# Optimization experiments

Measured on AMD Instinct MI355X. Metric: run time of the kernel, lower is better.

Reference implementation:

```python
import jax, jax.numpy as jnp
import numpy as np

B, N, D, DA = 8, 2048, 512, 64


def setup_inputs() -> dict:
    key = jax.random.key(0)
    ks = jax.random.split(key, 10)
    s = 1.0 / np.sqrt(D)
    return {
        "x": jax.random.normal(ks[0], (B, N, D), jnp.float32),
        "query_aux": jax.random.normal(ks[1], (B, N, DA), jnp.float32),
        "key_aux": jax.random.normal(ks[2], (B, N, DA), jnp.float32),
        "adjacency_mask": jax.random.randint(ks[3], (B, N, N), 0, 2, jnp.int32),
        "merge_coefficients": jax.random.uniform(ks[4], (1,), jnp.float32),
        "Wq": jax.random.normal(ks[5], (D, D), jnp.float32) * s,
        "bq": jnp.zeros((D,), jnp.float32),
        "Wk": jax.random.normal(ks[6], (D, D), jnp.float32) * s,
        "bk": jnp.zeros((D,), jnp.float32),
        "Wv": jax.random.normal(ks[7], (D, D), jnp.float32) * s,
        "bv": jnp.zeros((D,), jnp.float32),
        "threshold": jnp.float32(0.5),
    }


def reference(x, query_aux, key_aux, adjacency_mask, merge_coefficients,
              Wq, bq, Wk, bk, Wv, bv, threshold):
    d_model = Wq.shape[0]
    scale = jnp.asarray(d_model, x.dtype) ** 0.5
    # torch nn.Linear: y = x @ W.T + b
    q = jnp.einsum('bnd,ed->bne', x, Wq) + bq
    k = jnp.einsum('bnd,ed->bne', x, Wk) + bk
    v = jnp.einsum('bnd,ed->bne', x, Wv) + bv

    scores = jnp.einsum('bne,bme->bnm', q, k) / scale  # [B,N,N]

    aux_scale = jnp.asarray(key_aux.shape[-1], x.dtype) ** 0.5
    scores_aux = jnp.einsum('bna,bma->bnm', query_aux, key_aux) / aux_scale

    merge_mask = (scores_aux != 0) & (scores > threshold)
    c = merge_coefficients
    merged = (1.0 - c) * scores + c * scores_aux
    scores = jnp.where(merge_mask, merged, scores)

    mask_value = jnp.finfo(scores.dtype).min
    scores = jnp.where(adjacency_mask == 0, mask_value, scores)

    weights = jax.nn.softmax(scores, axis=-1)
    return jnp.einsum('bnm,bme->bne', weights, v)
```

## Files before the change

### kernel.cpp

```cpp
#include <hip/hip_runtime.h>
#include <cstdint>

typedef _Float16 f16;
typedef _Float16 f16x4 __attribute__((ext_vector_type(4)));
typedef _Float16 f16x8 __attribute__((ext_vector_type(8)));
typedef float    f32x4 __attribute__((ext_vector_type(4)));

#define MFMA(a,b,c) __builtin_amdgcn_mfma_f32_16x16x32_f16((a),(b),(c),0,0,0)

constexpr int  Bb = 8, Nn = 2048, Dd = 512, Ad = 64;
constexpr long XN = (long)Bb*Nn*Dd;
constexpr long WN = (long)Dd*Dd;
constexpr long AN = (long)Bb*Nn*Ad;
constexpr float LO_S  = 4096.f;
constexpr float LO_INV= 1.f/4096.f;
constexpr float P_SC  = 1024.f;
constexpr float NEGF  = -3.402823466e38f;

__global__ void prep_split(const float* __restrict__ x,
  const float* __restrict__ Wq, const float* __restrict__ Wk, const float* __restrict__ Wv,
  const float* __restrict__ aq, const float* __restrict__ ak,
  f16* __restrict__ xh, f16* __restrict__ xl, f16* __restrict__ Wh, f16* __restrict__ Wl,
  f16* __restrict__ aqh, f16* __restrict__ akh)
{
  const long total4 = (XN + 3*WN + 2*AN) >> 2;
  for (long u = blockIdx.x*(long)blockDim.x + threadIdx.x; u < total4;
       u += (long)gridDim.x*blockDim.x) {
    long i = u << 2;
    if (i < XN) {
      float4 v = *(const float4*)(x + i);
      float vv[4] = {v.x, v.y, v.z, v.w};
      f16x4 h, l;
      #pragma unroll
      for (int t=0;t<4;++t){ f16 hh=(f16)vv[t]; h[t]=hh; l[t]=(f16)((vv[t]-(float)hh)*LO_S); }
      *(f16x4*)(xh+i)=h; *(f16x4*)(xl+i)=l;
    } else if (i < XN + 3*WN) {
      long j = i - XN;
      const float* w = (j < WN) ? (Wq + j) : (j < 2*WN ? (Wk + (j-WN)) : (Wv + (j-2*WN)));
      float4 v = *(const float4*)w;
      float vv[4] = {v.x, v.y, v.z, v.w};
      f16x4 h, l;
      #pragma unroll
      for (int t=0;t<4;++t){ f16 hh=(f16)vv[t]; h[t]=hh; l[t]=(f16)((vv[t]-(float)hh)*LO_S); }
      *(f16x4*)(Wh+j)=h; *(f16x4*)(Wl+j)=l;
    } else {
      long j = i - XN - 3*WN;
      const float* s = (j < AN) ? (aq + j) : (ak + (j-AN));
      f16*         d = (j < AN) ? (aqh + j) : (akh + (j-AN));
      float4 v = *(const float4*)s;
      float vv[4] = {v.x, v.y, v.z, v.w};
      f16x4 h;
      #pragma unroll
      for (int t=0;t<4;++t) h[t]=(f16)vv[t];
      *(f16x4*)d = h;
    }
  }
}

__global__ __launch_bounds__(256, 2) void proj_qk(
  const f16* __restrict__ xh, const f16* __restrict__ xl,
  const f16* __restrict__ Wh, const f16* __restrict__ Wl,
  const float* __restrict__ bq, const float* __restrict__ bk,
  f16* __restrict__ qh, f16* __restrict__ ql,
  f16* __restrict__ kh, f16* __restrict__ kl)
{
  const int z = blockIdx.z;
  const f16* Whz = Wh + (long)z*WN;
  const f16* Wlz = Wl + (long)z*WN;
  const float* bias = z ? bk : bq;
  f16* oh = z ? kh : qh;
  f16* ol = z ? kl : ql;
  const int e0 = blockIdx.x*128, m0 = blockIdx.y*128;
  __shared__ f16 Ah[128][40], Al[128][40], Bh[128][40], Bl[128][40];
  const int tid = threadIdx.x, lane = tid & 63, wid = tid >> 6;
  const int wi = wid & 1, wj = wid >> 1;
  const int r16 = lane & 15, g16 = lane >> 4;

  f32x4 acch[4][4], accl[4][4];
  #pragma unroll
  for (int a=0;a<4;++a)
    #pragma unroll
    for (int bI=0;bI<4;++bI){ acch[a][bI]=(f32x4){0.f,0.f,0.f,0.f}; accl[a][bI]=(f32x4){0.f,0.f,0.f,0.f}; }

  f16x8 st[8];
  #pragma unroll
  for (int t=0;t<2;++t) {
    int u = tid + t*256; int row = u>>2, sg = u&3;
    long ko = (long)sg*8;
    st[t*4+0] = *(const f16x8*)&Whz[(long)(e0+row)*Dd + ko];
    st[t*4+1] = *(const f16x8*)&Wlz[(long)(e0+row)*Dd + ko];
    st[t*4+2] = *(const f16x8*)&xh [(long)(m0+row)*Dd + ko];
    st[t*4+3] = *(const f16x8*)&xl [(long)(m0+row)*Dd + ko];
  }
  for (int kt=0; kt<16; ++kt) {
    __syncthreads();
    #pragma unroll
    for (int t=0;t<2;++t) {
      int u = tid + t*256; int row = u>>2, sg = u&3;
      *(f16x8*)&Ah[row][sg*8] = st[t*4+0];
      *(f16x8*)&Al[row][sg*8] = st[t*4+1];
      *(f16x8*)&Bh[row][sg*8] = st[t*4+2];
      *(f16x8*)&Bl[row][sg*8] = st[t*4+3];
    }
    __syncthreads();
    if (kt < 15) {
      #pragma unroll
      for (int t=0;t<2;++t) {
        int u = tid + t*256; int row = u>>2, sg = u&3;
        long ko = (long)(kt+1)*32 + sg*8;
        st[t*4+0] = *(const f16x8*)&Whz[(long)(e0+row)*Dd + ko];
        st[t*4+1] = *(const f16x8*)&Wlz[(long)(e0+row)*Dd + ko];
        st[t*4+2] = *(const f16x8*)&xh [(long)(m0+row)*Dd + ko];
        st[t*4+3] = *(const f16x8*)&xl [(long)(m0+row)*Dd + ko];
      }
    }
    f16x8 ahf[4], alf[4];
    #pragma unroll
    for (int fi=0;fi<4;++fi) {
      ahf[fi] = *(const f16x8*)&Ah[wi*64 + fi*16 + r16][g16*8];
      alf[fi] = *(const f16x8*)&Al[wi*64 + fi*16 + r16][g16*8];
    }
    #pragma unroll
    for (int fj=0;fj<4;++fj) {
      f16x8 bhf = *(const f16x8*)&Bh[wj*64 + fj*16 + r16][g16*8];
      f16x8 blf = *(const f16x8*)&Bl[wj*64 + fj*16 + r16][g16*8];
      #pragma unroll
      for (int fi=0;fi<4;++fi) {
        acch[fi][fj] = MFMA(ahf[fi], bhf, acch[fi][fj]);
        accl[fi][fj] = MFMA(ahf[fi], blf, accl[fi][fj]);
        accl[fi][fj] = MFMA(alf[fi], bhf, accl[fi][fj]);
      }
    }
  }
  #pragma unroll
  for (int fi=0;fi<4;++fi) {
    const int eb = e0 + wi*64 + fi*16 + g16*4;
    const float4 b4 = *(const float4*)&bias[eb];
    const float bbv[4] = {b4.x, b4.y, b4.z, b4.w};
    #pragma unroll
    for (int fj=0;fj<4;++fj) {
      const int xr = m0 + wj*64 + fj*16 + r16;
      f16x4 h4, l4;
      #pragma unroll
      for (int rg=0;rg<4;++rg) {
        float v = acch[fi][fj][rg] + accl[fi][fj][rg]*LO_INV + bbv[rg];
        f16 hh = (f16)v;
        h4[rg] = hh;
        l4[rg] = (f16)((v - (float)hh)*LO_S);
      }
      *(f16x4*)&oh[(long)xr*Dd + eb] = h4;
      *(f16x4*)&ol[(long)xr*Dd + eb] = l4;
    }
  }
}

__global__ __launch_bounds__(256, 2) void proj_v(
  const f16* __restrict__ xh, const f16* __restrict__ Wvh,
  const float* __restrict__ bv, f16* __restrict__ vT)
{
  const int e0 = blockIdx.x*128, m0 = blockIdx.y*128;
  __shared__ f16 Ax[128][40], Bw[128][40];
  const int tid = threadIdx.x, lane = tid & 63, wid = tid >> 6;
  const int wi = wid & 1, wj = wid >> 1;
  const int r16 = lane & 15, g16 = lane >> 4;

  f32x4 acc[4][4];
  #pragma unroll
  for (int a=0;a<4;++a)
    #pragma unroll
    for (int bI=0;bI<4;++bI) acc[a][bI]=(f32x4){0.f,0.f,0.f,0.f};

  f16x8 st[4];
  #pragma unroll
  for (int t=0;t<2;++t) {
    int u = tid + t*256; int row = u>>2, sg = u&3;
    st[t*2+0] = *(const f16x8*)&xh [(long)(m0+row)*Dd + sg*8];
    st[t*2+1] = *(const f16x8*)&Wvh[(long)(e0+row)*Dd + sg*8];
  }
  for (int kt=0; kt<16; ++kt) {
    __syncthreads();
    #pragma unroll
    for (int t=0;t<2;++t) {
      int u = tid + t*256; int row = u>>2, sg = u&3;
      *(f16x8*)&Ax[row][sg*8] = st[t*2+0];
      *(f16x8*)&Bw[row][sg*8] = st[t*2+1];
    }
    __syncthreads();
    if (kt < 15) {
      #pragma unroll
      for (int t=0;t<2;++t) {
        int u = tid + t*256; int row = u>>2, sg = u&3;
        long ko = (long)(kt+1)*32 + sg*8;
        st[t*2+0] = *(const f16x8*)&xh [(long)(m0+row)*Dd + ko];
        st[t*2+1] = *(const f16x8*)&Wvh[(long)(e0+row)*Dd + ko];
      }
    }
    f16x8 af[4];
    #pragma unroll
    for (int fi=0;fi<4;++fi) af[fi] = *(const f16x8*)&Ax[wi*64 + fi*16 + r16][g16*8];
    #pragma unroll
    for (int fj=0;fj<4;++fj) {
      f16x8 bf = *(const f16x8*)&Bw[wj*64 + fj*16 + r16][g16*8];
      #pragma unroll
      for (int fi=0;fi<4;++fi) acc[fi][fj] = MFMA(af[fi], bf, acc[fi][fj]);
    }
  }
  #pragma unroll
  for (int fj=0;fj<4;++fj) {
    const int e = e0 + wj*64 + fj*16 + r16;
    const float bve = bv[e];
    #pragma unroll
    for (int fi=0;fi<4;++fi) {
      const int xr0 = m0 + wi*64 + fi*16 + g16*4;
      const int bbi = xr0 >> 11, nn = xr0 & 2047;
      f16x4 h4;
      #pragma unroll
      for (int rg=0;rg<4;++rg) h4[rg] = (f16)(acc[fi][fj][rg] + bve);
      *(f16x4*)&vT[((long)bbi*Dd + e)*Nn + nn] = h4;
    }
  }
}

constexpr int FLASH_LDS = 121856;

__global__ __launch_bounds__(512, 2) void flash(
  const f16* __restrict__ qhg, const f16* __restrict__ qlg,
  const f16* __restrict__ khg, const f16* __restrict__ klg,
  const f16* __restrict__ vT,  const f16* __restrict__ aqg, const f16* __restrict__ akg,
  const int* __restrict__ adj, const float* __restrict__ mcp, const float* __restrict__ thp,
  float* __restrict__ out)
{
  extern __shared__ char smem[];
  f16 (* __restrict__ QL)[520] = (f16(*)[520])(smem);
  f16 (* __restrict__ KH)[136] = (f16(*)[136])(smem + 66560);
  f16 (* __restrict__ KL)[136] = (f16(*)[136])(smem + 83968);
  f16 (* __restrict__ AK)[72]  = (f16(*)[72]) (smem + 101376);
  f16 (* __restrict__ PS)[72]  = (f16(*)[72]) (smem + 110592);
  float* pmax = (float*)(smem + 119808);
  float* psum = (float*)(smem + 120320);
  float* mnew = (float*)(smem + 120832);
  float* scl  = (float*)(smem + 121088);
  float* mst  = (float*)(smem + 121344);
  float* lst  = (float*)(smem + 121600);

  const int b  = blockIdx.y;
  const int r0 = blockIdx.x * 64;
  const int tid = threadIdx.x;
  const int lane = tid & 63, wid = tid >> 6;
  const int wm = wid & 3, wn = wid >> 2;
  const int r16 = lane & 15, g16 = lane >> 4;
  const float cc = mcp[0], thr = thp[0];

  if (tid < 64) { mst[tid] = NEGF; lst[tid] = 0.f; }

  const long qbase = ((long)(b*Nn + r0))*Dd;
  for (int u = tid; u < 64*Dd/8; u += 512) {
    int row = u >> 6, sg = u & 63;
    *(f16x8*)&QL[row][sg*8] = *(const f16x8*)&qlg[qbase + (long)row*Dd + sg*8];
  }
  f16x8 qhr[16];
  {
    const f16* qrow = qhg + qbase + (long)(wm*16 + r16)*Dd;
    #pragma unroll
    for (int ks=0; ks<16; ++ks) qhr[ks] = *(const f16x8*)&qrow[ks*32 + g16*8];
  }
  f16x8 aqr[2];
  {
    const f16* arow = aqg + ((long)(b*Nn + r0 + wm*16 + r16))*Ad;
    aqr[0] = *(const f16x8*)&arow[g16*8];
    aqr[1] = *(const f16x8*)&arow[32 + g16*8];
  }
  f32x4 oacc[4][4];
  #pragma unroll
  for (int i=0;i<4;++i)
    #pragma unroll
    for (int j=0;j<4;++j) oacc[i][j] = (f32x4){0.f,0.f,0.f,0.f};

  __syncthreads();

  for (int ct=0; ct<Nn/64; ++ct) {
    const int cb = ct*64;
    int adjv[2][4];
    {
      const int* ap = adj + ((long)(b*Nn + r0 + wm*16))*Nn + cb + wn*32 + r16;
      #pragma unroll
      for (int nf=0; nf<2; ++nf)
        #pragma unroll
        for (int rg=0; rg<4; ++rg)
          adjv[nf][rg] = ap[(long)(g16*4+rg)*Nn + nf*16];
    }
    f32x4 sacc[2], slo[2], aacc[2];
    #pragma unroll
    for (int nf=0;nf<2;++nf){ sacc[nf]=(f32x4){0.f,0.f,0.f,0.f}; slo[nf]=(f32x4){0.f,0.f,0.f,0.f}; aacc[nf]=(f32x4){0.f,0.f,0.f,0.f}; }

    for (int kc=0; kc<4; ++kc) {
      __syncthreads();
      {
        const long gb = ((long)(b*Nn + cb))*Dd + kc*128;
        const int ua = tid, ub = tid + 512;
        const int ra = ua>>4, sa = ua&15, rb = ub>>4, sb = ub&15;
        f16x8 h0 = *(const f16x8*)&khg[gb + (long)ra*Dd + sa*8];
        f16x8 h1 = *(const f16x8*)&khg[gb + (long)rb*Dd + sb*8];
        f16x8 l0 = *(const f16x8*)&klg[gb + (long)ra*Dd + sa*8];
        f16x8 l1 = *(const f16x8*)&klg[gb + (long)rb*Dd + sb*8];
        *(f16x8*)&KH[ra][sa*8] = h0;
        *(f16x8*)&KH[rb][sb*8] = h1;
        *(f16x8*)&KL[ra][sa*8] = l0;
        *(f16x8*)&KL[rb][sb*8] = l1;
        if (kc == 3) {
          int rr = tid>>3, sg = tid&7;
          *(f16x8*)&AK[rr][sg*8] = *(const f16x8*)&akg[((long)(b*Nn + cb))*Ad + (long)rr*Ad + sg*8];
        }
      }
      __syncthreads();
      #pragma unroll
      for (int k4=0; k4<4; ++k4) {
        const int ks = kc*4 + k4;
        f16x8 alo = *(const f16x8*)&QL[wm*16 + r16][ks*32 + g16*8];
        #pragma unroll
        for (int nf=0; nf<2; ++nf) {
          const int cr = wn*32 + nf*16 + r16;
          f16x8 bh = *(const f16x8*)&KH[cr][k4*32 + g16*8];
          f16x8 bl = *(const f16x8*)&KL[cr][k4*32 + g16*8];
          sacc[nf] = MFMA(qhr[ks], bh, sacc[nf]);
          slo[nf]  = MFMA(qhr[ks], bl, slo[nf]);
          slo[nf]  = MFMA(alo,     bh, slo[nf]);
        }
      }
    }
    #pragma unroll
    for (int ks=0; ks<2; ++ks)
      #pragma unroll
      for (int nf=0; nf<2; ++nf) {
        f16x8 bf = *(const f16x8*)&AK[wn*32 + nf*16 + r16][ks*32 + g16*8];
        aacc[nf] = MFMA(aqr[ks], bf, aacc[nf]);
      }
    float sv[2][4], mx[4];
    #pragma unroll
    for (int rg=0; rg<4; ++rg) {
      #pragma unroll
      for (int nf=0; nf<2; ++nf) {
        float s = (sacc[nf][rg] + slo[nf][rg]*LO_INV) / 22.627416997969522f;
        float a = aacc[nf][rg] * 0.125f;
        float m = (1.f - cc)*s + cc*a;
        s = ((a != 0.f) && (s > thr)) ? m : s;
        sv[nf][rg] = adjv[nf][rg] ? s : NEGF;
      }
      mx[rg] = fmaxf(sv[0][rg], sv[1][rg]);
    }
    #pragma unroll
    for (int off=1; off<16; off<<=1)
      #pragma unroll
      for (int rg=0; rg<4; ++rg)
        mx[rg] = fmaxf(mx[rg], __shfl_xor(mx[rg], off));
    if (r16 == 0) {
      #pragma unroll
      for (int rg=0; rg<4; ++rg) pmax[wn*64 + wm*16 + g16*4 + rg] = mx[rg];
    }
    __syncthreads();
    if (tid < 64) {
      float tmax = fmaxf(pmax[tid], pmax[64+tid]);
      float mo = mst[tid];
      float mn = fmaxf(mo, tmax);
      mnew[tid] = mn;
      scl[tid]  = expf(mo - mn);
      mst[tid]  = mn;
    }
    __syncthreads();
    float sm[4];
    #pragma unroll
    for (int rg=0; rg<4; ++rg) {
      const int rr = wm*16 + g16*4 + rg;
      const float mn = mnew[rr];
      float p0 = expf(sv[0][rg] - mn);
      float p1 = expf(sv[1][rg] - mn);
      PS[rr][wn*32 + r16]      = (f16)(p0 * P_SC);
      PS[rr][wn*32 + 16 + r16] = (f16)(p1 * P_SC);
      sm[rg] = p0 + p1;
    }
    #pragma unroll
    for (int off=1; off<16; off<<=1)
      #pragma unroll
      for (int rg=0; rg<4; ++rg)
        sm[rg] += __shfl_xor(sm[rg], off);
    if (r16 == 0) {
      #pragma unroll
      for (int rg=0; rg<4; ++rg) psum[wn*64 + wm*16 + g16*4 + rg] = sm[rg];
    }
    __syncthreads();
    if (tid < 64) lst[tid] = lst[tid]*scl[tid] + psum[tid] + psum[64+tid];
    float scj[4];
    #pragma unroll
    for (int j=0;j<4;++j) scj[j] = scl[j*16 + r16];
    #pragma unroll
    for (int i=0;i<4;++i)
      #pragma unroll
      for (int j=0;j<4;++j)
        #pragma unroll
        for (int rg=0;rg<4;++rg) oacc[i][j][rg] *= scj[j];
    #pragma unroll
    for (int ks=0; ks<2; ++ks) {
      f16x8 va[4];
      const f16* vb = vT + ((long)(b*Dd) + wid*64 + r16)*Nn + cb + ks*32 + g16*8;
      #pragma unroll
      for (int i=0;i<4;++i) va[i] = *(const f16x8*)&vb[(long)i*16*Nn];
      #pragma unroll
      for (int j=0;j<4;++j) {
        f16x8 pb = *(const f16x8*)&PS[j*16 + r16][ks*32 + g16*8];
        #pragma unroll
        for (int i=0;i<4;++i) oacc[i][j] = MFMA(va[i], pb, oacc[i][j]);
      }
    }
  }
  __syncthreads();
  const long ob = ((long)(b*Nn + r0))*Dd;
  #pragma unroll
  for (int j=0;j<4;++j) {
    const int rr = j*16 + r16;
    const float li = 1.f / (lst[rr] * P_SC);
    #pragma unroll
    for (int i=0;i<4;++i) {
      f32x4 v;
      #pragma unroll
      for (int rg=0;rg<4;++rg) v[rg] = oacc[i][j][rg] * li;
      *(f32x4*)&out[ob + (long)rr*Dd + wid*64 + i*16 + g16*4] = v;
    }
  }
}

extern "C" void kernel_launch(void* const* d_in, const int* in_sizes, int n_in,
                              void* d_out, int out_size, void* d_ws, size_t ws_size,
                              hipStream_t stream)
{
  const float* x   = (const float*)d_in[0];
  const float* qa  = (const float*)d_in[1];
  const float* ka  = (const float*)d_in[2];
  const int*   adj = (const int*)  d_in[3];
  const float* mc  = (const float*)d_in[4];
  const float* Wq  = (const float*)d_in[5];
  const float* bq  = (const float*)d_in[6];
  const float* Wk  = (const float*)d_in[7];
  const float* bk  = (const float*)d_in[8];
  const float* Wv  = (const float*)d_in[9];
  const float* bv  = (const float*)d_in[10];
  const float* th  = (const float*)d_in[11];
  float* out = (float*)d_out;

  f16* p  = (f16*)d_ws;
  f16* xh = p;  p += XN;
  f16* xl = p;  p += XN;
  f16* Wh = p;  p += 3*WN;
  f16* Wl = p;  p += 3*WN;
  f16* qh = p;  p += XN;
  f16* ql = p;  p += XN;
  f16* kh = p;  p += XN;
  f16* kl = p;  p += XN;
  f16* vT = p;  p += XN;
  f16* aqh = p; p += AN;
  f16* akh = p; p += AN;

  prep_split<<<dim3(2048), dim3(256), 0, stream>>>(x, Wq, Wk, Wv, qa, ka,
                                                   xh, xl, Wh, Wl, aqh, akh);
  proj_qk<<<dim3(4,128,2), dim3(256), 0, stream>>>(xh, xl, Wh, Wl, bq, bk,
                                                   qh, ql, kh, kl);
  proj_v<<<dim3(4,128), dim3(256), 0, stream>>>(xh, Wh + 2*WN, bv, vT);

  hipFuncSetAttribute(reinterpret_cast<const void*>(flash),
                      hipFuncAttributeMaxDynamicSharedMemorySize, FLASH_LDS);
  flash<<<dim3(Nn/64, Bb), dim3(512), FLASH_LDS, stream>>>(qh, ql, kh, kl, vT,
                                                           aqh, akh, adj, mc, th, out);
}
```

Before: 431.6 us.

## Double-buffer K tiles with register prefetch and swizzled LDS in flash kernel

Prefetches the next K hi/lo chunk into registers during MFMA work and writes it to a second LDS buffer, halving barriers per chunk. Replaces padded LDS arrays with XOR-swizzled layouts, hoists V loads before the softmax, raises wave priority around MFMA blocks, and uses fast exp. The grid is flattened with batch interleaving. Higher LDS use and register pressure may limit occupancy.

```diff
diff --git a/kernel.cpp b/kernel.cpp
--- a/kernel.cpp
+++ b/kernel.cpp
@@ -16,6 +16,9 @@
 constexpr float LO_INV= 1.f/4096.f;
 constexpr float P_SC  = 1024.f;
 constexpr float NEGF  = -3.402823466e38f;
+
+#define QSWZ(row, cb2) ((row)*1024 + ((cb2) ^ (((row)&7)<<4)))
+#define KSWZ(row, cb2) ((row)*256  + ((cb2) ^ (((row)&7)<<4)))
 
 __global__ void prep_split(const float* __restrict__ x,
   const float* __restrict__ Wq, const float* __restrict__ Wk, const float* __restrict__ Wv,
@@ -221,7 +224,7 @@
   }
 }
 
-constexpr int FLASH_LDS = 121856;
+constexpr int FLASH_LDS = 151552;
 
 __global__ __launch_bounds__(512, 2) void flash(
   const f16* __restrict__ qhg, const f16* __restrict__ qlg,
@@ -231,42 +234,47 @@
   float* __restrict__ out)
 {
   extern __shared__ char smem[];
-  f16 (* __restrict__ QL)[520] = (f16(*)[520])(smem);
-  f16 (* __restrict__ KH)[136] = (f16(*)[136])(smem + 66560);
-  f16 (* __restrict__ KL)[136] = (f16(*)[136])(smem + 83968);
-  f16 (* __restrict__ AK)[72]  = (f16(*)[72]) (smem + 101376);
-  f16 (* __restrict__ PS)[72]  = (f16(*)[72]) (smem + 110592);
-  float* pmax = (float*)(smem + 119808);
-  float* psum = (float*)(smem + 120320);
-  float* mnew = (float*)(smem + 120832);
-  float* scl  = (float*)(smem + 121088);
-  float* mst  = (float*)(smem + 121344);
-  float* lst  = (float*)(smem + 121600);
-
-  const int b  = blockIdx.y;
-  const int r0 = blockIdx.x * 64;
+  char* QLb = smem;
+  char* KHb0 = smem + 65536;
+  char* KHb1 = smem + 81920;
+  char* KLb0 = smem + 98304;
+  char* KLb1 = smem + 114688;
+  f16 (* __restrict__ AK)[72] = (f16(*)[72])(smem + 131072);
+  f16 (* __restrict__ PS)[72] = (f16(*)[72])(smem + 140288);
+  float* pmax = (float*)(smem + 149504);
+  float* psum = pmax + 128;
+  float* mnew = psum + 128;
+  float* scl  = mnew + 64;
+  float* mst  = scl + 64;
+  float* lst  = mst + 64;
+
+  const int bid = blockIdx.x;
+  const int b   = bid & 7;
+  const int r0  = (bid >> 3) * 64;
   const int tid = threadIdx.x;
   const int lane = tid & 63, wid = tid >> 6;
   const int wm = wid & 3, wn = wid >> 2;
   const int r16 = lane & 15, g16 = lane >> 4;
+  const int g16c = g16 * 16;
+  const int qrow = wm*16 + r16;
   const float cc = mcp[0], thr = thp[0];
 
   if (tid < 64) { mst[tid] = NEGF; lst[tid] = 0.f; }
 
   const long qbase = ((long)(b*Nn + r0))*Dd;
-  for (int u = tid; u < 64*Dd/8; u += 512) {
+  for (int u = tid; u < 4096; u += 512) {
     int row = u >> 6, sg = u & 63;
-    *(f16x8*)&QL[row][sg*8] = *(const f16x8*)&qlg[qbase + (long)row*Dd + sg*8];
+    *(f16x8*)(QLb + QSWZ(row, sg*16)) = *(const f16x8*)&qlg[qbase + (long)row*Dd + sg*8];
   }
   f16x8 qhr[16];
   {
-    const f16* qrow = qhg + qbase + (long)(wm*16 + r16)*Dd;
-    #pragma unroll
-    for (int ks=0; ks<16; ++ks) qhr[ks] = *(const f16x8*)&qrow[ks*32 + g16*8];
+    const f16* qrp = qhg + qbase + (long)qrow*Dd;
+    #pragma unroll
+    for (int ks=0; ks<16; ++ks) qhr[ks] = *(const f16x8*)&qrp[ks*32 + g16*8];
   }
   f16x8 aqr[2];
   {
-    const f16* arow = aqg + ((long)(b*Nn + r0 + wm*16 + r16))*Ad;
+    const f16* arow = aqg + ((long)(b*Nn + r0 + qrow))*Ad;
     aqr[0] = *(const f16x8*)&arow[g16*8];
     aqr[1] = *(const f16x8*)&arow[32 + g16*8];
   }
@@ -276,6 +284,22 @@
     #pragma unroll
     for (int j=0;j<4;++j) oacc[i][j] = (f32x4){0.f,0.f,0.f,0.f};
 
+  const int crow = tid >> 4, csl = tid & 15;
+  const int wo0 = KSWZ(crow,      csl*16);
+  const int wo1 = KSWZ(crow + 32, csl*16);
+  f16x8 skh0, skh1, skl0, skl1, sak;
+
+  {
+    const long gb = ((long)(b*Nn))*Dd;
+    skh0 = *(const f16x8*)&khg[gb + (long)crow*Dd      + csl*8];
+    skh1 = *(const f16x8*)&khg[gb + (long)(crow+32)*Dd + csl*8];
+    skl0 = *(const f16x8*)&klg[gb + (long)crow*Dd      + csl*8];
+    skl1 = *(const f16x8*)&klg[gb + (long)(crow+32)*Dd + csl*8];
+    *(f16x8*)(KHb0 + wo0) = skh0;
+    *(f16x8*)(KHb0 + wo1) = skh1;
+    *(f16x8*)(KLb0 + wo0) = skl0;
+    *(f16x8*)(KLb0 + wo1) = skl1;
+  }
   __syncthreads();
 
   for (int ct=0; ct<Nn/64; ++ct) {
@@ -294,39 +318,47 @@
     for (int nf=0;nf<2;++nf){ sacc[nf]=(f32x4){0.f,0.f,0.f,0.f}; slo[nf]=(f32x4){0.f,0.f,0.f,0.f}; aacc[nf]=(f32x4){0.f,0.f,0.f,0.f}; }
 
     for (int kc=0; kc<4; ++kc) {
-      __syncthreads();
-      {
-        const long gb = ((long)(b*Nn + cb))*Dd + kc*128;
-        const int ua = tid, ub = tid + 512;
-        const int ra = ua>>4, sa = ua&15, rb = ub>>4, sb = ub&15;
-        f16x8 h0 = *(const f16x8*)&khg[gb + (long)ra*Dd + sa*8];
-        f16x8 h1 = *(const f16x8*)&khg[gb + (long)rb*Dd + sb*8];
-        f16x8 l0 = *(const f16x8*)&klg[gb + (long)ra*Dd + sa*8];
-        f16x8 l1 = *(const f16x8*)&klg[gb + (long)rb*Dd + sb*8];
-        *(f16x8*)&KH[ra][sa*8] = h0;
-        *(f16x8*)&KH[rb][sb*8] = h1;
-        *(f16x8*)&KL[ra][sa*8] = l0;
-        *(f16x8*)&KL[rb][sb*8] = l1;
-        if (kc == 3) {
-          int rr = tid>>3, sg = tid&7;
-          *(f16x8*)&AK[rr][sg*8] = *(const f16x8*)&akg[((long)(b*Nn + cb))*Ad + (long)rr*Ad + sg*8];
-        }
-      }
-      __syncthreads();
+      const int slot = ct*4 + kc;
+      char* KHc = (slot & 1) ? KHb1 : KHb0;
+      char* KLc = (slot & 1) ? KLb1 : KLb0;
+      char* KHn = (slot & 1) ? KHb0 : KHb1;
+      char* KLn = (slot & 1) ? KLb0 : KLb1;
+      if (slot < 127) {
+        const int ns = slot + 1;
+        const long gb = ((long)(b*Nn + (ns>>2)*64))*Dd + (ns&3)*128;
+        skh0 = *(const f16x8*)&khg[gb + (long)crow*Dd      + csl*8];
+        skh1 = *(const f16x8*)&khg[gb + (long)(crow+32)*Dd + csl*8];
+        skl0 = *(const f16x8*)&klg[gb + (long)crow*Dd      + csl*8];
+        skl1 = *(const f16x8*)&klg[gb + (long)(crow+32)*Dd + csl*8];
+      }
+      if (kc == 2)
+        sak = *(const f16x8*)&akg[((long)(b*Nn + cb))*Ad + (long)(tid>>3)*Ad + (tid&7)*8];
+
+      __builtin_amdgcn_s_setprio(1);
       #pragma unroll
       for (int k4=0; k4<4; ++k4) {
         const int ks = kc*4 + k4;
-        f16x8 alo = *(const f16x8*)&QL[wm*16 + r16][ks*32 + g16*8];
+        f16x8 alo = *(const f16x8*)(QLb + QSWZ(qrow, ks*64 + g16c));
         #pragma unroll
         for (int nf=0; nf<2; ++nf) {
           const int cr = wn*32 + nf*16 + r16;
-          f16x8 bh = *(const f16x8*)&KH[cr][k4*32 + g16*8];
-          f16x8 bl = *(const f16x8*)&KL[cr][k4*32 + g16*8];
+          f16x8 bh = *(const f16x8*)(KHc + KSWZ(cr, k4*64 + g16c));
+          f16x8 bl = *(const f16x8*)(KLc + KSWZ(cr, k4*64 + g16c));
           sacc[nf] = MFMA(qhr[ks], bh, sacc[nf]);
           slo[nf]  = MFMA(qhr[ks], bl, slo[nf]);
           slo[nf]  = MFMA(alo,     bh, slo[nf]);
         }
       }
+      __builtin_amdgcn_s_setprio(0);
+
+      if (slot < 127) {
+        *(f16x8*)(KHn + wo0) = skh0;
+        *(f16x8*)(KHn + wo1) = skh1;
+        *(f16x8*)(KLn + wo0) = skl0;
+        *(f16x8*)(KLn + wo1) = skl1;
+      }
+      if (kc == 2) *(f16x8*)&AK[tid>>3][(tid&7)*8] = sak;
+      __syncthreads();
     }
     #pragma unroll
     for (int ks=0; ks<2; ++ks)
@@ -335,6 +367,15 @@
         f16x8 bf = *(const f16x8*)&AK[wn*32 + nf*16 + r16][ks*32 + g16*8];
         aacc[nf] = MFMA(aqr[ks], bf, aacc[nf]);
       }
+    f16x8 va[2][4];
+    {
+      const f16* vb = vT + ((long)(b*Dd) + wid*64 + r16)*Nn + cb;
+      #pragma unroll
+      for (int ks=0; ks<2; ++ks)
+        #pragma unroll
+        for (int i=0;i<4;++i)
+          va[ks][i] = *(const f16x8*)&vb[(long)i*16*Nn + ks*32 + g16*8];
+    }
     float sv[2][4], mx[4];
     #pragma unroll
     for (int rg=0; rg<4; ++rg) {
@@ -363,7 +404,7 @@
       float mo = mst[tid];
       float mn = fmaxf(mo, tmax);
       mnew[tid] = mn;
-      scl[tid]  = expf(mo - mn);
+      scl[tid]  = __expf(mo - mn);
       mst[tid]  = mn;
     }
     __syncthreads();
@@ -372,8 +413,8 @@
     for (int rg=0; rg<4; ++rg) {
       const int rr = wm*16 + g16*4 + rg;
       const float mn = mnew[rr];
-      float p0 = expf(sv[0][rg] - mn);
-      float p1 = expf(sv[1][rg] - mn);
+      float p0 = __expf(sv[0][rg] - mn);
+      float p1 = __expf(sv[1][rg] - mn);
       PS[rr][wn*32 + r16]      = (f16)(p0 * P_SC);
       PS[rr][wn*32 + 16 + r16] = (f16)(p1 * P_SC);
       sm[rg] = p0 + p1;
@@ -398,19 +439,17 @@
       for (int j=0;j<4;++j)
         #pragma unroll
         for (int rg=0;rg<4;++rg) oacc[i][j][rg] *= scj[j];
+    __builtin_amdgcn_s_setprio(1);
     #pragma unroll
     for (int ks=0; ks<2; ++ks) {
-      f16x8 va[4];
-      const f16* vb = vT + ((long)(b*Dd) + wid*64 + r16)*Nn + cb + ks*32 + g16*8;
-      #pragma unroll
-      for (int i=0;i<4;++i) va[i] = *(const f16x8*)&vb[(long)i*16*Nn];
       #pragma unroll
       for (int j=0;j<4;++j) {
         f16x8 pb = *(const f16x8*)&PS[j*16 + r16][ks*32 + g16*8];
         #pragma unroll
-        for (int i=0;i<4;++i) oacc[i][j] = MFMA(va[i], pb, oacc[i][j]);
-      }
-    }
+        for (int i=0;i<4;++i) oacc[i][j] = MFMA(va[ks][i], pb, oacc[i][j]);
+      }
+    }
+    __builtin_amdgcn_s_setprio(0);
   }
   __syncthreads();
   const long ob = ((long)(b*Nn + r0))*Dd;
@@ -467,6 +506,6 @@
 
   hipFuncSetAttribute(reinterpret_cast<const void*>(flash),
                       hipFuncAttributeMaxDynamicSharedMemorySize, FLASH_LDS);
-  flash<<<dim3(Nn/64, Bb), dim3(512), FLASH_LDS, stream>>>(qh, ql, kh, kl, vT,
-                                                           aqh, akh, adj, mc, th, out);
+  flash<<<dim3(256), dim3(512), FLASH_LDS, stream>>>(qh, ql, kh, kl, vT,
+                                                     aqh, akh, adj, mc, th, out);
 }
```

New measurement: 611.0 us. 41.6% more time.
